# Performance work log

Measured on AMD Instinct MI355X. Metric: run time of the kernel, lower is better.

The kernel has to match this reference:

```python
import jax, jax.numpy as jnp
import numpy as np

KEY_DIM, VALUE_DIM, N_ACTIONS = 128, 64, 256
B, L = 32, 2048


def setup_inputs() -> dict:
    key = jax.random.key(0)
    k1, k2, k3 = jax.random.split(key, 3)
    key_vectors = jax.random.normal(k1, (B, L, KEY_DIM), dtype=jnp.float32)
    value_vectors = jax.random.normal(k2, (B, N_ACTIONS, KEY_DIM), dtype=jnp.float32)
    weights = jax.random.normal(k3, (KEY_DIM, VALUE_DIM, N_ACTIONS), dtype=jnp.float32)
    return {"key_vectors": key_vectors, "value_vectors": value_vectors, "weights": weights}


def reference(key_vectors, value_vectors, weights):
    # torch: einsum('bln,nka->bla', key, W) sums over both n (key_dim) and k (value_dim)
    scores = jnp.einsum('bln,nka->bla', key_vectors, weights)  # (B, L, A)
    # fused multiply-then-reduce over actions == batched matmul (no (B,L,A,D) intermediate)
    mem_vectors = jnp.einsum('bla,bad->bld', scores, value_vectors)  # (B, L, key_dim)
    q_values = jnp.einsum('bln,bmn->blm', key_vectors, mem_vectors)  # (B, L, L)
    return q_values
```

## Files before the change

### kernel.cpp

```cpp
#include <hip/hip_runtime.h>
#include <hip/hip_bf16.h>

#define KD 128
#define VD 64
#define NA 256
#define NB 32
#define LL 2048

typedef __attribute__((ext_vector_type(8))) short bf16x8;
typedef __attribute__((ext_vector_type(4))) float f32x4;
typedef __attribute__((ext_vector_type(8))) unsigned short u16x8;
typedef __attribute__((ext_vector_type(4))) unsigned short u16x4;

static __device__ __forceinline__ unsigned short f2bf(float x) {
  __hip_bfloat16 h = __float2bfloat16(x);
  unsigned short u;
  __builtin_memcpy(&u, &h, 2);
  return u;
}

static __device__ __forceinline__ void stage16(const void* gsrc, void* ldst) {
  __builtin_amdgcn_global_load_lds(
      (const __attribute__((address_space(1))) void*)gsrc,
      (__attribute__((address_space(3))) void*)ldst, 16, 0, 0);
}

__global__ __launch_bounds__(256) void fold_w(const float* __restrict__ W,
                                              float* __restrict__ W2) {
  const int idx = blockIdx.x * 256 + threadIdx.x;
  const int n = idx >> 8, a = idx & 255;
  const float* p = W + (long)n * (VD * NA) + a;
  float s = 0.f;
  #pragma unroll
  for (int k = 0; k < VD; ++k) s += p[k * NA];
  W2[idx] = s;
}

__global__ __launch_bounds__(128) void compute_t(const float* __restrict__ W2,
                                                 const float* __restrict__ V,
                                                 unsigned short* __restrict__ Tt) {
  const int n = threadIdx.x;
  const int d0 = blockIdx.x * 8;
  const int b = blockIdx.y;
  const float* vb = V + (long)b * NA * KD + d0;
  const float* w2p = W2 + n * NA;
  float acc[8] = {0.f, 0.f, 0.f, 0.f, 0.f, 0.f, 0.f, 0.f};
  for (int a = 0; a < NA; a += 4) {
    const float4 w = *(const float4*)(w2p + a);
    const float wq[4] = {w.x, w.y, w.z, w.w};
    #pragma unroll
    for (int q = 0; q < 4; ++q) {
      const float* vr = vb + (long)(a + q) * KD;
      #pragma unroll
      for (int j = 0; j < 8; ++j) acc[j] += wq[q] * vr[j];
    }
  }
  #pragma unroll
  for (int j = 0; j < 8; ++j)
    Tt[((long)b * KD + d0 + j) * KD + n] = f2bf(acc[j]);
}

__global__ __launch_bounds__(256) void cvt_key(const float* __restrict__ in,
                                               unsigned short* __restrict__ out) {
  const long i = ((long)blockIdx.x * 256 + threadIdx.x) * 8;
  const float4 f0 = *(const float4*)(in + i);
  const float4 f1 = *(const float4*)(in + i + 4);
  u16x8 r;
  r[0] = f2bf(f0.x); r[1] = f2bf(f0.y); r[2] = f2bf(f0.z); r[3] = f2bf(f0.w);
  r[4] = f2bf(f1.x); r[5] = f2bf(f1.y); r[6] = f2bf(f1.z); r[7] = f2bf(f1.w);
  *(u16x8*)(out + i) = r;
}

__global__ __launch_bounds__(256) void gemm_mem(const unsigned short* __restrict__ A,
                                                const unsigned short* __restrict__ Bm,
                                                unsigned short* __restrict__ C) {
  __shared__ unsigned short lds[32768];
  const int nper = gridDim.x >> 3;
  const int lg = (blockIdx.x & 7) * nper + (blockIdx.x >> 3);
  const int mt = lg & 15;
  const int b = lg >> 4;

  const int tid = threadIdx.x;
  const int lane = tid & 63, w = tid >> 6;
  const int l15 = lane & 15, lhi = lane >> 4;

  const unsigned short* gA = A + ((long)b * LL + mt * 128) * KD;
  const unsigned short* gB = Bm + (long)b * KD * KD;

  unsigned short* ldsA = lds;
  unsigned short* ldsB = lds + 16384;

  #pragma unroll
  for (int i = 0; i < 8; ++i) {
    const int addr = (w * 8 + i) * 1024 + lane * 16;
    const int row = addr >> 8;
    const int src = addr ^ ((row & 7) << 4);
    stage16((const char*)gA + src, (char*)ldsA + addr);
    stage16((const char*)gB + src, (char*)ldsB + addr);
  }
  __syncthreads();

  const int wr = w >> 1, wc = w & 1;
  f32x4 acc[4][4];
  #pragma unroll
  for (int i = 0; i < 4; ++i)
    #pragma unroll
    for (int j = 0; j < 4; ++j) acc[i][j] = f32x4{0.f, 0.f, 0.f, 0.f};

  #pragma unroll
  for (int ks = 0; ks < 4; ++ks) {
    const int kb = (ks * 32 + lhi * 8) * 2;
    bf16x8 av[4], bv[4];
    #pragma unroll
    for (int mf = 0; mf < 4; ++mf) {
      const int row = wr * 64 + mf * 16 + l15;
      const int byte = (row * 256 + kb) ^ ((row & 7) << 4);
      av[mf] = *(const bf16x8*)((const char*)ldsA + byte);
    }
    #pragma unroll
    for (int nf = 0; nf < 4; ++nf) {
      const int row = wc * 64 + nf * 16 + l15;
      const int byte = (row * 256 + kb) ^ ((row & 7) << 4);
      bv[nf] = *(const bf16x8*)((const char*)ldsB + byte);
    }
    #pragma unroll
    for (int mf = 0; mf < 4; ++mf)
      #pragma unroll
      for (int nf = 0; nf < 4; ++nf)
        acc[mf][nf] = __builtin_amdgcn_mfma_f32_16x16x32_bf16(bv[nf], av[mf],
                                                              acc[mf][nf], 0, 0, 0);
  }

  const long row0 = (long)b * LL + mt * 128 + wr * 64;
  const int col0 = wc * 64;
  #pragma unroll
  for (int mf = 0; mf < 4; ++mf)
    #pragma unroll
    for (int nf = 0; nf < 4; ++nf) {
      const long r = row0 + mf * 16 + l15;
      const int c = col0 + nf * 16 + lhi * 4;
      u16x4 v;
      #pragma unroll
      for (int i = 0; i < 4; ++i) v[i] = f2bf(acc[mf][nf][i]);
      *(u16x4*)(C + r * KD + c) = v;
    }
}

__global__ __launch_bounds__(512, 2) void gemm_q(const unsigned short* __restrict__ A,
                                                 const unsigned short* __restrict__ Bm,
                                                 float* __restrict__ C) {
  __shared__ unsigned short ldsA[32768];
  __shared__ unsigned short ldsB[32768];

  const int lg = (blockIdx.x & 7) * 32 + (blockIdx.x >> 3);
  const int nt = lg & 7;
  const int b = lg >> 3;

  const int tid = threadIdx.x;
  const int lane = tid & 63, w = tid >> 6;
  const int l15 = lane & 15, lhi = lane >> 4;
  const int wrM = w >> 2;
  const int wcN = w & 3;

  const unsigned short* gB = Bm + ((long)b * LL + nt * 256) * KD;
  const unsigned short* gAb = A + (long)b * LL * KD;

  #pragma unroll
  for (int i = 0; i < 8; ++i) {
    const int addr = i * 8192 + tid * 16;
    const int row = addr >> 8;
    const int src = addr ^ ((row & 7) << 4);
    stage16((const char*)gB + src, (char*)ldsB + addr);
    stage16((const char*)gAb + src, (char*)ldsA + addr);
  }
  asm volatile("s_waitcnt vmcnt(0)" ::: "memory");
  __builtin_amdgcn_s_barrier();
  __builtin_amdgcn_sched_barrier(0);

  const int col0 = nt * 256 + wcN * 64;

  for (int mt = 0; mt < 8; ++mt) {
    f32x4 acc[8][4];
    #pragma unroll
    for (int i = 0; i < 8; ++i)
      #pragma unroll
      for (int j = 0; j < 4; ++j) acc[i][j] = f32x4{0.f, 0.f, 0.f, 0.f};

    #pragma unroll
    for (int ks = 0; ks < 4; ++ks) {
      const int kb = (ks * 32 + lhi * 8) * 2;
      bf16x8 av[8], bv[4];
      #pragma unroll
      for (int mf = 0; mf < 8; ++mf) {
        const int row = wrM * 128 + mf * 16 + l15;
        const int byte = (row * 256 + kb) ^ ((row & 7) << 4);
        av[mf] = *(const bf16x8*)((const char*)ldsA + byte);
      }
      #pragma unroll
      for (int nf = 0; nf < 4; ++nf) {
        const int row = wcN * 64 + nf * 16 + l15;
        const int byte = (row * 256 + kb) ^ ((row & 7) << 4);
        bv[nf] = *(const bf16x8*)((const char*)ldsB + byte);
      }
      #pragma unroll
      for (int mf = 0; mf < 8; ++mf)
        #pragma unroll
        for (int nf = 0; nf < 4; ++nf)
          acc[mf][nf] = __builtin_amdgcn_mfma_f32_16x16x32_bf16(bv[nf], av[mf],
                                                                acc[mf][nf], 0, 0, 0);
    }

    asm volatile("s_waitcnt lgkmcnt(0)" ::: "memory");
    __builtin_amdgcn_s_barrier();
    __builtin_amdgcn_sched_barrier(0);

    if (mt < 7) {
      const char* gA = (const char*)(gAb + (long)(mt + 1) * 256 * KD);
      #pragma unroll
      for (int i = 0; i < 8; ++i) {
        const int addr = i * 8192 + tid * 16;
        const int row = addr >> 8;
        const int src = addr ^ ((row & 7) << 4);
        stage16(gA + src, (char*)ldsA + addr);
      }
    }
    __builtin_amdgcn_sched_barrier(0);

    const long row0 = (long)b * LL + mt * 256 + wrM * 128;
    #pragma unroll
    for (int mf = 0; mf < 8; ++mf)
      #pragma unroll
      for (int nf = 0; nf < 4; ++nf) {
        const long r = row0 + mf * 16 + l15;
        const int c = col0 + nf * 16 + lhi * 4;
        *(f32x4*)(C + r * LL + c) = acc[mf][nf];
      }

    if (mt < 7) {
      asm volatile("s_waitcnt vmcnt(32)" ::: "memory");
      __builtin_amdgcn_sched_barrier(0);
      __builtin_amdgcn_s_barrier();
      __builtin_amdgcn_sched_barrier(0);
    }
  }
}

extern "C" void kernel_launch(void* const* d_in, const int* in_sizes, int n_in,
                              void* d_out, int out_size, void* d_ws, size_t ws_size,
                              hipStream_t stream) {
  const float* key = (const float*)d_in[0];
  const float* val = (const float*)d_in[1];
  const float* wts = (const float*)d_in[2];
  float* out = (float*)d_out;

  char* ws = (char*)d_ws;
  float* W2 = (float*)ws;
  unsigned short* Tt = (unsigned short*)(ws + 131072);
  unsigned short* keyB = (unsigned short*)(ws + 131072 + 1048576);
  unsigned short* memB = (unsigned short*)(ws + 131072 + 1048576 + 16777216);

  fold_w<<<128, 256, 0, stream>>>(wts, W2);
  compute_t<<<dim3(16, NB), 128, 0, stream>>>(W2, val, Tt);
  cvt_key<<<4096, 256, 0, stream>>>(key, keyB);
  gemm_mem<<<16 * NB, 256, 0, stream>>>(keyB, Tt, memB);
  gemm_q<<<8 * NB, 512, 0, stream>>>(keyB, memB, out);
}
```

Before: 165.5 us.

## Fuse key conversion into mem GEMM and double-buffer A tiles in q GEMM

The separate fp32-to-bf16 key conversion kernel is folded into the mem GEMM, which now converts key rows in registers, writes them to LDS and also stores the bf16 copy for the later GEMM. This saves one launch and one re-read of the bf16 key tile. In the q GEMM, the A tile is halved to 128 rows and split across two LDS buffers, so the next tile's load is issued before the current MFMA loop instead of after a barrier. The trade is smaller per-iteration work and twice as many loop iterations, with the output still write-bound.

```diff
diff --git a/kernel.cpp b/kernel.cpp
--- a/kernel.cpp
+++ b/kernel.cpp
@@ -60,21 +60,12 @@
     Tt[((long)b * KD + d0 + j) * KD + n] = f2bf(acc[j]);
 }
 
-__global__ __launch_bounds__(256) void cvt_key(const float* __restrict__ in,
-                                               unsigned short* __restrict__ out) {
-  const long i = ((long)blockIdx.x * 256 + threadIdx.x) * 8;
-  const float4 f0 = *(const float4*)(in + i);
-  const float4 f1 = *(const float4*)(in + i + 4);
-  u16x8 r;
-  r[0] = f2bf(f0.x); r[1] = f2bf(f0.y); r[2] = f2bf(f0.z); r[3] = f2bf(f0.w);
-  r[4] = f2bf(f1.x); r[5] = f2bf(f1.y); r[6] = f2bf(f1.z); r[7] = f2bf(f1.w);
-  *(u16x8*)(out + i) = r;
-}
-
-__global__ __launch_bounds__(256) void gemm_mem(const unsigned short* __restrict__ A,
-                                                const unsigned short* __restrict__ Bm,
-                                                unsigned short* __restrict__ C) {
-  __shared__ unsigned short lds[32768];
+__global__ __launch_bounds__(256) void gemm_mem_f(const float* __restrict__ key,
+                                                  const unsigned short* __restrict__ Tt,
+                                                  unsigned short* __restrict__ keyB,
+                                                  unsigned short* __restrict__ memB) {
+  __shared__ unsigned short ldsA[16384];
+  __shared__ unsigned short ldsB[16384];
   const int nper = gridDim.x >> 3;
   const int lg = (blockIdx.x & 7) * nper + (blockIdx.x >> 3);
   const int mt = lg & 15;
@@ -84,19 +75,30 @@
   const int lane = tid & 63, w = tid >> 6;
   const int l15 = lane & 15, lhi = lane >> 4;
 
-  const unsigned short* gA = A + ((long)b * LL + mt * 128) * KD;
-  const unsigned short* gB = Bm + (long)b * KD * KD;
-
-  unsigned short* ldsA = lds;
-  unsigned short* ldsB = lds + 16384;
+  const float* gK = key + ((long)b * LL + mt * 128) * KD;
+  unsigned short* gKB = keyB + ((long)b * LL + mt * 128) * KD;
+  const unsigned short* gB = Tt + (long)b * KD * KD;
 
   #pragma unroll
   for (int i = 0; i < 8; ++i) {
     const int addr = (w * 8 + i) * 1024 + lane * 16;
     const int row = addr >> 8;
     const int src = addr ^ ((row & 7) << 4);
-    stage16((const char*)gA + src, (char*)ldsA + addr);
     stage16((const char*)gB + src, (char*)ldsB + addr);
+  }
+  #pragma unroll
+  for (int it = 0; it < 8; ++it) {
+    const int idx = it * 256 + tid;
+    const int row = idx >> 4;
+    const int c8 = idx & 15;
+    const float4 f0 = *(const float4*)(gK + row * KD + c8 * 8);
+    const float4 f1 = *(const float4*)(gK + row * KD + c8 * 8 + 4);
+    u16x8 v;
+    v[0] = f2bf(f0.x); v[1] = f2bf(f0.y); v[2] = f2bf(f0.z); v[3] = f2bf(f0.w);
+    v[4] = f2bf(f1.x); v[5] = f2bf(f1.y); v[6] = f2bf(f1.z); v[7] = f2bf(f1.w);
+    *(u16x8*)(gKB + row * KD + c8 * 8) = v;
+    const int byte = (row * 256 + c8 * 16) ^ ((row & 7) << 4);
+    *(u16x8*)((char*)ldsA + byte) = v;
   }
   __syncthreads();
 
@@ -142,15 +144,16 @@
       u16x4 v;
       #pragma unroll
       for (int i = 0; i < 4; ++i) v[i] = f2bf(acc[mf][nf][i]);
-      *(u16x4*)(C + r * KD + c) = v;
+      *(u16x4*)(memB + r * KD + c) = v;
     }
 }
 
 __global__ __launch_bounds__(512, 2) void gemm_q(const unsigned short* __restrict__ A,
                                                  const unsigned short* __restrict__ Bm,
                                                  float* __restrict__ C) {
-  __shared__ unsigned short ldsA[32768];
   __shared__ unsigned short ldsB[32768];
+  __shared__ unsigned short ldsA0[16384];
+  __shared__ unsigned short ldsA1[16384];
 
   const int lg = (blockIdx.x & 7) * 32 + (blockIdx.x >> 3);
   const int nt = lg & 7;
@@ -171,7 +174,13 @@
     const int row = addr >> 8;
     const int src = addr ^ ((row & 7) << 4);
     stage16((const char*)gB + src, (char*)ldsB + addr);
-    stage16((const char*)gAb + src, (char*)ldsA + addr);
+  }
+  #pragma unroll
+  for (int i = 0; i < 4; ++i) {
+    const int addr = i * 8192 + tid * 16;
+    const int row = addr >> 8;
+    const int src = addr ^ ((row & 7) << 4);
+    stage16((const char*)gAb + src, (char*)ldsA0 + addr);
   }
   asm volatile("s_waitcnt vmcnt(0)" ::: "memory");
   __builtin_amdgcn_s_barrier();
@@ -179,22 +188,34 @@
 
   const int col0 = nt * 256 + wcN * 64;
 
-  for (int mt = 0; mt < 8; ++mt) {
-    f32x4 acc[8][4];
-    #pragma unroll
-    for (int i = 0; i < 8; ++i)
+  auto gen = [&](int mt, const unsigned short* abuf, unsigned short* nbuf) {
+    if (mt < 15) {
+      const char* gA = (const char*)(gAb + (long)(mt + 1) * 128 * KD);
+      #pragma unroll
+      for (int i = 0; i < 4; ++i) {
+        const int addr = i * 8192 + tid * 16;
+        const int row = addr >> 8;
+        const int src = addr ^ ((row & 7) << 4);
+        stage16(gA + src, (char*)nbuf + addr);
+      }
+    }
+    __builtin_amdgcn_sched_barrier(0);
+
+    f32x4 acc[4][4];
+    #pragma unroll
+    for (int i = 0; i < 4; ++i)
       #pragma unroll
       for (int j = 0; j < 4; ++j) acc[i][j] = f32x4{0.f, 0.f, 0.f, 0.f};
 
     #pragma unroll
     for (int ks = 0; ks < 4; ++ks) {
       const int kb = (ks * 32 + lhi * 8) * 2;
-      bf16x8 av[8], bv[4];
-      #pragma unroll
-      for (int mf = 0; mf < 8; ++mf) {
-        const int row = wrM * 128 + mf * 16 + l15;
+      bf16x8 av[4], bv[4];
+      #pragma unroll
+      for (int mf = 0; mf < 4; ++mf) {
+        const int row = wrM * 64 + mf * 16 + l15;
         const int byte = (row * 256 + kb) ^ ((row & 7) << 4);
-        av[mf] = *(const bf16x8*)((const char*)ldsA + byte);
+        av[mf] = *(const bf16x8*)((const char*)abuf + byte);
       }
       #pragma unroll
       for (int nf = 0; nf < 4; ++nf) {
@@ -203,32 +224,16 @@
         bv[nf] = *(const bf16x8*)((const char*)ldsB + byte);
       }
       #pragma unroll
-      for (int mf = 0; mf < 8; ++mf)
+      for (int mf = 0; mf < 4; ++mf)
         #pragma unroll
         for (int nf = 0; nf < 4; ++nf)
           acc[mf][nf] = __builtin_amdgcn_mfma_f32_16x16x32_bf16(bv[nf], av[mf],
                                                                 acc[mf][nf], 0, 0, 0);
     }
 
-    asm volatile("s_waitcnt lgkmcnt(0)" ::: "memory");
-    __builtin_amdgcn_s_barrier();
-    __builtin_amdgcn_sched_barrier(0);
-
-    if (mt < 7) {
-      const char* gA = (const char*)(gAb + (long)(mt + 1) * 256 * KD);
-      #pragma unroll
-      for (int i = 0; i < 8; ++i) {
-        const int addr = i * 8192 + tid * 16;
-        const int row = addr >> 8;
-        const int src = addr ^ ((row & 7) << 4);
-        stage16(gA + src, (char*)ldsA + addr);
-      }
-    }
-    __builtin_amdgcn_sched_barrier(0);
-
-    const long row0 = (long)b * LL + mt * 256 + wrM * 128;
-    #pragma unroll
-    for (int mf = 0; mf < 8; ++mf)
+    const long row0 = (long)b * LL + mt * 128 + wrM * 64;
+    #pragma unroll
+    for (int mf = 0; mf < 4; ++mf)
       #pragma unroll
       for (int nf = 0; nf < 4; ++nf) {
         const long r = row0 + mf * 16 + l15;
@@ -236,12 +241,18 @@
         *(f32x4*)(C + r * LL + c) = acc[mf][nf];
       }
 
-    if (mt < 7) {
-      asm volatile("s_waitcnt vmcnt(32)" ::: "memory");
+    if (mt < 15) {
+      asm volatile("s_waitcnt vmcnt(16)" ::: "memory");
       __builtin_amdgcn_sched_barrier(0);
       __builtin_amdgcn_s_barrier();
       __builtin_amdgcn_sched_barrier(0);
     }
+  };
+
+  #pragma unroll 1
+  for (int mt2 = 0; mt2 < 8; ++mt2) {
+    gen(2 * mt2, ldsA0, ldsA1);
+    gen(2 * mt2 + 1, ldsA1, ldsA0);
   }
 }
 
@@ -261,7 +272,6 @@
 
   fold_w<<<128, 256, 0, stream>>>(wts, W2);
   compute_t<<<dim3(16, NB), 128, 0, stream>>>(W2, val, Tt);
-  cvt_key<<<4096, 256, 0, stream>>>(key, keyB);
-  gemm_mem<<<16 * NB, 256, 0, stream>>>(keyB, Tt, memB);
+  gemm_mem_f<<<16 * NB, 256, 0, stream>>>(key, Tt, keyB, memB);
   gemm_q<<<8 * NB, 512, 0, stream>>>(keyB, memB, out);
 }
```

New measurement: 159.5 us. 3.6% less time.
